# Kernel optimization log

Measured on AMD Instinct MI355X. Metric: run time of the kernel, lower is better.

## Reference

```python
import jax, jax.numpy as jnp
import numpy as np
from jax import lax

EPS = 1e-5  # BatchNorm3d default eps


def _dwconv3d(x, w, pad):
    # x: [N,C,D,H,W], w: [C,1,k,k,k] depthwise kernel
    C = w.shape[0]
    return lax.conv_general_dilated(
        x, w,
        window_strides=(1, 1, 1),
        padding=[(pad, pad)] * 3,
        dimension_numbers=('NCDHW', 'OIDHW', 'NCDHW'),
        feature_group_count=C,
    )


def _bn_relu(y, gamma, beta, mean, var):
    # Inference-mode BatchNorm3d folded into a per-channel affine, then ReLU.
    inv = gamma / jnp.sqrt(var + EPS)          # [C]
    scale = inv.reshape(1, -1, 1, 1, 1)
    bias = (beta - mean * inv).reshape(1, -1, 1, 1, 1)
    return jax.nn.relu(y * scale + bias)


def setup_inputs() -> dict:
    key = jax.random.key(0)
    ks = jax.random.split(key, 20)
    C = 32
    x = jax.random.normal(ks[0], (2, C, 64, 128, 128), dtype=jnp.float32)
    w7 = jax.random.normal(ks[1], (C, 1, 7, 7, 7), dtype=jnp.float32) * 0.05
    w3 = jax.random.normal(ks[2], (C, 1, 3, 3, 3), dtype=jnp.float32) * 0.1
    w1 = jax.random.normal(ks[3], (C, 1, 1, 1, 1), dtype=jnp.float32) * 0.3
    def bn_params(i):
        g = jax.random.normal(ks[4 + 4 * i], (C,), dtype=jnp.float32) * 0.1 + 1.0
        b = jax.random.normal(ks[5 + 4 * i], (C,), dtype=jnp.float32) * 0.1
        m = jax.random.normal(ks[6 + 4 * i], (C,), dtype=jnp.float32) * 0.1
        v = jax.random.uniform(ks[7 + 4 * i], (C,), dtype=jnp.float32) + 0.5
        return g, b, m, v
    g7, b7, m7, v7 = bn_params(0)
    g3, b3, m3, v3 = bn_params(1)
    g1, b1, m1, v1 = bn_params(2)
    return dict(x=x, w7=w7, w3=w3, w1=w1,
                g7=g7, b7=b7, m7=m7, v7=v7,
                g3=g3, b3=b3, m3=m3, v3=v3,
                g1=g1, b1=b1, m1=m1, v1=v1)


def reference(x, w7, w3, w1,
              g7, b7, m7, v7,
              g3, b3, m3, v3,
              g1, b1, m1, v1):
    # y = relu(bn7(dw7(x))) + relu(bn3(dw3(x))) + relu(bn1(dw1(x)))
    y = _bn_relu(_dwconv3d(x, w7, 3), g7, b7, m7, v7)
    y = y + _bn_relu(_dwconv3d(x, w3, 1), g3, b3, m3, v3)
    # 1x1x1 depthwise conv == per-channel scalar multiply
    y = y + _bn_relu(x * w1[:, 0, 0, 0, 0].reshape(1, -1, 1, 1, 1), g1, b1, m1, v1)
    return jax.nn.relu(x + y)
```

## Files before the change

### kernel.cpp

```cpp
#include <hip/hip_runtime.h>
#include <hip/hip_bf16.h>

#define Dd 64
#define Hh 128
#define Ww 128
#define Cc 32

#define BD 32
#define BH 16
#define BW 16
#define ZR (BD + 6)
#define HR (BH + 6)
#define NR (ZR * HR)
#define RCOLS 24
#define BLKROW 3
#define NBLK (NR * BLKROW)

#define N7WIN 14
#define N3WIN 10
#define W3BASE (49 * N7WIN)
#define ZENT   (W3BASE + 9 * N3WIN)
#define NENT   (ZENT + 1)

typedef __attribute__((ext_vector_type(8))) short short8;
typedef __attribute__((ext_vector_type(4))) float floatx4;

static __device__ __forceinline__ unsigned short f2bf(float f) {
    unsigned u = __builtin_bit_cast(unsigned, f);
    u += 0x7fffu + ((u >> 16) & 1u);
    return (unsigned short)(u >> 16);
}

static __device__ __forceinline__ unsigned pk2(float a, float b) {
    union { __hip_bfloat162 h; unsigned u; } cv;
    cv.h = __float22bfloat162_rn(make_float2(a, b));
    return cv.u;
}

__global__ __launch_bounds__(256, 3) void replk_mfma(
    const float* __restrict__ x,
    const float* __restrict__ w7, const float* __restrict__ w3, const float* __restrict__ w1,
    const float* __restrict__ g7, const float* __restrict__ b7, const float* __restrict__ m7, const float* __restrict__ v7,
    const float* __restrict__ g3, const float* __restrict__ b3, const float* __restrict__ m3, const float* __restrict__ v3,
    const float* __restrict__ g1, const float* __restrict__ b1, const float* __restrict__ m1, const float* __restrict__ v1,
    float* __restrict__ out)
{
    __shared__ __align__(16) unsigned short tile[NR * RCOLS];
    __shared__ __align__(16) unsigned short wtab[NENT * 8];

    const int tid = threadIdx.x;

    const unsigned lid = blockIdx.x;
    const unsigned nl = (lid & 7u) * 1024u + (lid >> 3);
    const int bx = nl & 127;
    const int slab = nl >> 7;
    const int c = slab & 31;
    const int nb = slab >> 5;
    const int w0 = (bx & 7) * BW;
    const int h0 = ((bx >> 3) & 7) * BH;
    const int d0 = (bx >> 6) * BD;

    const float* xc = x + (size_t)(nb * Cc + c) * (Dd * Hh * Ww);

    for (int e = tid; e < NENT; e += 256) {
        unsigned short h8[8];
#pragma unroll
        for (int j = 0; j < 8; j++) {
            float v = 0.f;
            if (e < W3BASE) {
                int pl = e / N7WIN, a = e - pl * N7WIN;
                int t = a + j - 7;
                if ((unsigned)t < 7u)
                    v = w7[c * 343 + (pl / 7) * 49 + (pl % 7) * 7 + t];
            } else if (e < ZENT) {
                int e2 = e - W3BASE;
                int p3 = e2 / N3WIN, a = e2 - p3 * N3WIN;
                int t = a + j - 7;
                if ((unsigned)t < 3u)
                    v = w3[c * 27 + (p3 / 3) * 9 + (p3 % 3) * 3 + t];
            }
            h8[j] = f2bf(v);
        }
        uint4 pk;
        pk.x = (unsigned)h8[0] | ((unsigned)h8[1] << 16);
        pk.y = (unsigned)h8[2] | ((unsigned)h8[3] << 16);
        pk.z = (unsigned)h8[4] | ((unsigned)h8[5] << 16);
        pk.w = (unsigned)h8[6] | ((unsigned)h8[7] << 16);
        *(uint4*)&wtab[e * 8] = pk;
    }

#pragma unroll
    for (int it = 0; it < 10; it++) {
        int s = tid + it * 256;
        if (s < NBLK) {
            int R = s / BLKROW, bl = s - R * BLKROW;
            int zi = R / HR, hr = R - zi * HR;
            int gz = d0 - 3 + zi, gh = h0 - 3 + hr, gw0 = w0 - 4 + bl * 8;
            float v[8];
#pragma unroll
            for (int j = 0; j < 8; j++) v[j] = 0.f;
            if ((unsigned)gz < (unsigned)Dd && (unsigned)gh < (unsigned)Hh) {
                const float* src = xc + ((size_t)gz * Hh + gh) * Ww + gw0;
                if (gw0 >= 0 && gw0 + 8 <= Ww) {
                    float4 a = *(const float4*)src;
                    float4 b = *(const float4*)(src + 4);
                    v[0] = a.x; v[1] = a.y; v[2] = a.z; v[3] = a.w;
                    v[4] = b.x; v[5] = b.y; v[6] = b.z; v[7] = b.w;
                } else {
#pragma unroll
                    for (int j = 0; j < 8; j++) {
                        int gw = gw0 + j;
                        if ((unsigned)gw < (unsigned)Ww) v[j] = src[j];
                    }
                }
            }
            uint4 pk;
            pk.x = pk2(v[0], v[1]);
            pk.y = pk2(v[2], v[3]);
            pk.z = pk2(v[4], v[5]);
            pk.w = pk2(v[6], v[7]);
            *(uint4*)&tile[R * RCOLS + bl * 8] = pk;
        }
    }

    const float eps = 1e-5f;
    const float iv7 = g7[c] / sqrtf(v7[c] + eps);
    const float bb7 = b7[c] - m7[c] * iv7;
    const float iv3 = g3[c] / sqrtf(v3[c] + eps);
    const float bb3 = b3[c] - m3[c] * iv3;
    const float iv1 = g1[c] / sqrtf(v1[c] + eps);
    const float bb1 = b1[c] - m1[c] * iv1;
    const float s1 = w1[c] * iv1;

    __syncthreads();

    const int lane = tid & 63;
    const int wave = tid >> 6;
    const int q = lane & 15;
    const int p = lane >> 4;
    const int khp = p >> 1;
    const int kb  = p & 1;
    const int ddl = q >> 3;
    const int mwq = q & 7;
    const int zbase = wave * 8;

    const int a7 = 8 * kb - mwq + 6;
    const int a3 = a7 - 2;
    const short8* wf = (const short8*)wtab;

    floatx4 acc7[4][2], acc3[4][2];
#pragma unroll
    for (int i = 0; i < 4; i++)
#pragma unroll
        for (int wh = 0; wh < 2; wh++) { acc7[i][wh] = (floatx4)0.f; acc3[i][wh] = (floatx4)0.f; }

#pragma unroll 1
    for (int khg = 0; khg < 4; khg++) {
        const int kh = 2 * khg + khp;
        const bool ok7 = ((unsigned)a7 < 14u) && (kh <= 6);
        const int cb7 = ok7 ? (kh * 14 + a7 - ddl * 98) : (int)ZENT;
        const int st7 = ok7 ? 98 : 0;
        short8 A7g[8];
#pragma unroll
        for (int rz = 0; rz < 8; rz++) {
            int idx = cb7 + rz * st7;
            if (rz == 0) idx = (ddl == 0 && ok7) ? idx : (int)ZENT;
            if (rz == 7) idx = (ddl == 1 && ok7) ? idx : (int)ZENT;
            A7g[rz] = wf[idx];
        }

        const bool has3 = (khg == 1) || (khg == 2);
        short8 A3g[4] = {};
        if (has3) {
            const int kh3 = 2 * (khg - 1) + khp;
            const bool ok3 = ((unsigned)a3 < 10u) && (kh3 <= 2);
            const int cb3 = ok3 ? (W3BASE + kh3 * 10 + a3 - ddl * 30) : (int)ZENT;
            const int st3 = ok3 ? 30 : 0;
#pragma unroll
            for (int rz = 0; rz < 4; rz++) {
                int idx = cb3 + rz * st3;
                if (rz == 0) idx = (ddl == 0 && ok3) ? idx : (int)ZENT;
                if (rz == 3) idx = (ddl == 1 && ok3) ? idx : (int)ZENT;
                A3g[rz] = wf[idx];
            }
        }

        const int rowadd = (khg == 3) ? 6 : (2 * khg + khp);

#pragma unroll
        for (int zi = 0; zi < 14; zi++) {
            const int R = (zbase + zi) * HR + q + rowadd;
            const unsigned short* bp = &tile[R * RCOLS + 8 * kb];
            short8 B0 = *(const short8*)bp;
            short8 B1 = *(const short8*)(bp + 8);
#pragma unroll
            for (int ddg = 0; ddg < 4; ddg++) {
                const int rz = zi - 2 * ddg;
                if (rz >= 0 && rz < 8) {
                    acc7[ddg][0] = __builtin_amdgcn_mfma_f32_16x16x32_bf16(
                        A7g[rz], B0, acc7[ddg][0], 0, 0, 0);
                    acc7[ddg][1] = __builtin_amdgcn_mfma_f32_16x16x32_bf16(
                        A7g[rz], B1, acc7[ddg][1], 0, 0, 0);
                }
            }
            if (has3) {
#pragma unroll
                for (int ddg = 0; ddg < 4; ddg++) {
                    const int rz3 = zi - 2 - 2 * ddg;
                    if (rz3 >= 0 && rz3 < 4) {
                        acc3[ddg][0] = __builtin_amdgcn_mfma_f32_16x16x32_bf16(
                            A3g[rz3], B0, acc3[ddg][0], 0, 0, 0);
                        acc3[ddg][1] = __builtin_amdgcn_mfma_f32_16x16x32_bf16(
                            A3g[rz3], B1, acc3[ddg][1], 0, 0, 0);
                    }
                }
            }
        }
    }

#pragma unroll
    for (int ddg = 0; ddg < 4; ddg++) {
#pragma unroll
        for (int wh = 0; wh < 2; wh++) {
            const int d = d0 + zbase + 2 * ddg + khp;
            const int Rr = (zbase + 2 * ddg + khp + 3) * HR + (q + 3);
            uint2 u = *(const uint2*)&tile[Rr * RCOLS + 8 * wh + 4 * kb + 4];
            float xr[4];
            xr[0] = __builtin_bit_cast(float, u.x << 16);
            xr[1] = __builtin_bit_cast(float, u.x & 0xffff0000u);
            xr[2] = __builtin_bit_cast(float, u.y << 16);
            xr[3] = __builtin_bit_cast(float, u.y & 0xffff0000u);

            float2 dummy;
            size_t off = ((size_t)(nb * Cc + c) * Dd + d) * (Hh * Ww)
                       + (size_t)(h0 + q) * Ww + w0 + 8 * wh + 4 * kb;
            float o[4];
#pragma unroll
            for (int r = 0; r < 4; r++) {
                float y7 = fmaxf(fmaf(acc7[ddg][wh][r], iv7, bb7), 0.f);
                float y3 = fmaxf(fmaf(acc3[ddg][wh][r], iv3, bb3), 0.f);
                float y1 = fmaxf(fmaf(xr[r], s1, bb1), 0.f);
                o[r] = fmaxf(xr[r] + y7 + y3 + y1, 0.f);
            }
            *(float4*)(out + off) = make_float4(o[0], o[1], o[2], o[3]);
        }
    }
}

extern "C" void kernel_launch(void* const* d_in, const int* in_sizes, int n_in,
                              void* d_out, int out_size, void* d_ws, size_t ws_size,
                              hipStream_t stream) {
    const float* x  = (const float*)d_in[0];
    const float* w7 = (const float*)d_in[1];
    const float* w3 = (const float*)d_in[2];
    const float* w1 = (const float*)d_in[3];
    const float* g7 = (const float*)d_in[4];
    const float* b7 = (const float*)d_in[5];
    const float* m7 = (const float*)d_in[6];
    const float* v7 = (const float*)d_in[7];
    const float* g3 = (const float*)d_in[8];
    const float* b3 = (const float*)d_in[9];
    const float* m3 = (const float*)d_in[10];
    const float* v3 = (const float*)d_in[11];
    const float* g1 = (const float*)d_in[12];
    const float* b1 = (const float*)d_in[13];
    const float* m1 = (const float*)d_in[14];
    const float* v1 = (const float*)d_in[15];
    float* out = (float*)d_out;

    dim3 grid(8192);
    dim3 block(256);
    hipLaunchKernelGGL(replk_mfma, grid, block, 0, stream,
                       x, w7, w3, w1, g7, b7, m7, v7, g3, b3, m3, v3,
                       g1, b1, m1, v1, out);
}
```

Baseline: 260.5 us.

## Handle last kh row with K=16 MFMA instead of padded K=32 pass

The fourth kh-group iteration, which previously ran full 16x16x32 MFMAs with half the lanes contributing zero weights (kh=7 padding), is replaced by a dedicated pass using 16x16x16 bf16 MFMAs that cover only the kh=6 row. This removes wasted MFMA work on padded zero taps. The tile-load loop also replaces per-iteration divisions with incremental index updates, and weight packing uses the hardware bf16 pack conversion. Inline asm MFMA may limit compiler scheduling.

```diff
diff --git a/kernel.cpp b/kernel.cpp
--- a/kernel.cpp
+++ b/kernel.cpp
@@ -23,13 +23,8 @@
 #define NENT   (ZENT + 1)
 
 typedef __attribute__((ext_vector_type(8))) short short8;
+typedef __attribute__((ext_vector_type(4))) short short4v;
 typedef __attribute__((ext_vector_type(4))) float floatx4;
-
-static __device__ __forceinline__ unsigned short f2bf(float f) {
-    unsigned u = __builtin_bit_cast(unsigned, f);
-    u += 0x7fffu + ((u >> 16) & 1u);
-    return (unsigned short)(u >> 16);
-}
 
 static __device__ __forceinline__ unsigned pk2(float a, float b) {
     union { __hip_bfloat162 h; unsigned u; } cv;
@@ -63,63 +58,71 @@
     const float* xc = x + (size_t)(nb * Cc + c) * (Dd * Hh * Ww);
 
     for (int e = tid; e < NENT; e += 256) {
-        unsigned short h8[8];
+        float v[8];
 #pragma unroll
         for (int j = 0; j < 8; j++) {
-            float v = 0.f;
+            float vv = 0.f;
             if (e < W3BASE) {
                 int pl = e / N7WIN, a = e - pl * N7WIN;
                 int t = a + j - 7;
                 if ((unsigned)t < 7u)
-                    v = w7[c * 343 + (pl / 7) * 49 + (pl % 7) * 7 + t];
+                    vv = w7[c * 343 + (pl / 7) * 49 + (pl % 7) * 7 + t];
             } else if (e < ZENT) {
                 int e2 = e - W3BASE;
                 int p3 = e2 / N3WIN, a = e2 - p3 * N3WIN;
                 int t = a + j - 7;
                 if ((unsigned)t < 3u)
-                    v = w3[c * 27 + (p3 / 3) * 9 + (p3 % 3) * 3 + t];
-            }
-            h8[j] = f2bf(v);
+                    vv = w3[c * 27 + (p3 / 3) * 9 + (p3 % 3) * 3 + t];
+            }
+            v[j] = vv;
         }
         uint4 pk;
-        pk.x = (unsigned)h8[0] | ((unsigned)h8[1] << 16);
-        pk.y = (unsigned)h8[2] | ((unsigned)h8[3] << 16);
-        pk.z = (unsigned)h8[4] | ((unsigned)h8[5] << 16);
-        pk.w = (unsigned)h8[6] | ((unsigned)h8[7] << 16);
+        pk.x = pk2(v[0], v[1]);
+        pk.y = pk2(v[2], v[3]);
+        pk.z = pk2(v[4], v[5]);
+        pk.w = pk2(v[6], v[7]);
         *(uint4*)&wtab[e * 8] = pk;
     }
 
-#pragma unroll
-    for (int it = 0; it < 10; it++) {
-        int s = tid + it * 256;
-        if (s < NBLK) {
-            int R = s / BLKROW, bl = s - R * BLKROW;
-            int zi = R / HR, hr = R - zi * HR;
-            int gz = d0 - 3 + zi, gh = h0 - 3 + hr, gw0 = w0 - 4 + bl * 8;
-            float v[8];
-#pragma unroll
-            for (int j = 0; j < 8; j++) v[j] = 0.f;
-            if ((unsigned)gz < (unsigned)Dd && (unsigned)gh < (unsigned)Hh) {
-                const float* src = xc + ((size_t)gz * Hh + gh) * Ww + gw0;
-                if (gw0 >= 0 && gw0 + 8 <= Ww) {
-                    float4 a = *(const float4*)src;
-                    float4 b = *(const float4*)(src + 4);
-                    v[0] = a.x; v[1] = a.y; v[2] = a.z; v[3] = a.w;
-                    v[4] = b.x; v[5] = b.y; v[6] = b.z; v[7] = b.w;
-                } else {
-#pragma unroll
-                    for (int j = 0; j < 8; j++) {
-                        int gw = gw0 + j;
-                        if ((unsigned)gw < (unsigned)Ww) v[j] = src[j];
+    {
+        int s = tid;
+        int R = tid / 3;
+        int bl = tid - R * 3;
+        int zi = R / HR;
+        int hr = R - zi * HR;
+#pragma unroll
+        for (int it = 0; it < 10; it++) {
+            if (s < NBLK) {
+                int gz = d0 - 3 + zi, gh = h0 - 3 + hr, gw0 = w0 - 4 + bl * 8;
+                float v[8];
+#pragma unroll
+                for (int j = 0; j < 8; j++) v[j] = 0.f;
+                if ((unsigned)gz < (unsigned)Dd && (unsigned)gh < (unsigned)Hh) {
+                    const float* src = xc + ((size_t)gz * Hh + gh) * Ww + gw0;
+                    if (gw0 >= 0 && gw0 + 8 <= Ww) {
+                        float4 a = *(const float4*)src;
+                        float4 b = *(const float4*)(src + 4);
+                        v[0] = a.x; v[1] = a.y; v[2] = a.z; v[3] = a.w;
+                        v[4] = b.x; v[5] = b.y; v[6] = b.z; v[7] = b.w;
+                    } else {
+#pragma unroll
+                        for (int j = 0; j < 8; j++) {
+                            int gw = gw0 + j;
+                            if ((unsigned)gw < (unsigned)Ww) v[j] = src[j];
+                        }
                     }
                 }
-            }
-            uint4 pk;
-            pk.x = pk2(v[0], v[1]);
-            pk.y = pk2(v[2], v[3]);
-            pk.z = pk2(v[4], v[5]);
-            pk.w = pk2(v[6], v[7]);
-            *(uint4*)&tile[R * RCOLS + bl * 8] = pk;
+                uint4 pk;
+                pk.x = pk2(v[0], v[1]);
+                pk.y = pk2(v[2], v[3]);
+                pk.z = pk2(v[4], v[5]);
+                pk.w = pk2(v[6], v[7]);
+                *(uint4*)&tile[R * RCOLS + bl * 8] = pk;
+            }
+            s += 256;
+            bl += 1; R += 85; zi += 3; hr += 19;
+            if (bl == 3) { bl = 0; R += 1; hr += 1; }
+            if (hr >= HR) { hr -= HR; zi += 1; }
         }
     }
 
@@ -155,9 +158,9 @@
         for (int wh = 0; wh < 2; wh++) { acc7[i][wh] = (floatx4)0.f; acc3[i][wh] = (floatx4)0.f; }
 
 #pragma unroll 1
-    for (int khg = 0; khg < 4; khg++) {
+    for (int khg = 0; khg < 3; khg++) {
         const int kh = 2 * khg + khp;
-        const bool ok7 = ((unsigned)a7 < 14u) && (kh <= 6);
+        const bool ok7 = (unsigned)a7 < 14u;
         const int cb7 = ok7 ? (kh * 14 + a7 - ddl * 98) : (int)ZENT;
         const int st7 = ok7 ? 98 : 0;
         short8 A7g[8];
@@ -185,7 +188,7 @@
             }
         }
 
-        const int rowadd = (khg == 3) ? 6 : (2 * khg + khp);
+        const int rowadd = 2 * khg + khp;
 
 #pragma unroll
         for (int zi = 0; zi < 14; zi++) {
@@ -218,6 +221,38 @@
         }
     }
 
+    {
+        const int a16 = 4 * p - mwq + 6;
+        const bool okA = (unsigned)a16 < 14u;
+        const int cb6 = okA ? (6 * 14 + a16 - ddl * 98) : (int)ZENT;
+        const int st6 = okA ? 98 : 0;
+        short4v A6[8];
+#pragma unroll
+        for (int rz = 0; rz < 8; rz++) {
+            int idx = cb6 + rz * st6;
+            if (rz == 0) idx = (ddl == 0 && okA) ? idx : (int)ZENT;
+            if (rz == 7) idx = (ddl == 1 && okA) ? idx : (int)ZENT;
+            A6[rz] = *(const short4v*)&wtab[idx * 8];
+        }
+#pragma unroll
+        for (int zi = 0; zi < 14; zi++) {
+            const int R = (zbase + zi) * HR + q + 6;
+            const unsigned short* bp = &tile[R * RCOLS + 4 * p];
+            short4v B0 = *(const short4v*)bp;
+            short4v B1 = *(const short4v*)(bp + 8);
+#pragma unroll
+            for (int ddg = 0; ddg < 4; ddg++) {
+                const int rz = zi - 2 * ddg;
+                if (rz >= 0 && rz < 8) {
+                    asm("v_mfma_f32_16x16x16_bf16 %0, %1, %2, %0"
+                        : "+v"(acc7[ddg][0]) : "v"(A6[rz]), "v"(B0));
+                    asm("v_mfma_f32_16x16x16_bf16 %0, %1, %2, %0"
+                        : "+v"(acc7[ddg][1]) : "v"(A6[rz]), "v"(B1));
+                }
+            }
+        }
+    }
+
 #pragma unroll
     for (int ddg = 0; ddg < 4; ddg++) {
 #pragma unroll
@@ -231,7 +266,6 @@
             xr[2] = __builtin_bit_cast(float, u.y << 16);
             xr[3] = __builtin_bit_cast(float, u.y & 0xffff0000u);
 
-            float2 dummy;
             size_t off = ((size_t)(nb * Cc + c) * Dd + d) * (Hh * Ww)
                        + (size_t)(h0 + q) * Ww + w0 + 8 * wh + 4 * kb;
             float o[4];
```

Result: slower. 309.9 us (+18.9%).
